# Optimization experiments

Measured on AMD Instinct MI355X. Metric: run time of the kernel, lower is better.

## Reference

```python
import jax, jax.numpy as jnp
import numpy as np

B, C, D, H, W = 2, 128, 16, 16, 16
NH = 4
HD = C // NH
GROUPS = 32
EPS = 1e-5


def group_norm(x, w, b):
    # x: [B, C, D, H, W]; normalize over (C/GROUPS, D, H, W) per group
    Bb, Cc = x.shape[0], x.shape[1]
    xr = x.reshape(Bb, GROUPS, -1)
    mu = xr.mean(axis=-1, keepdims=True)
    var = xr.var(axis=-1, keepdims=True)
    xn = ((xr - mu) * jax.lax.rsqrt(var + EPS)).reshape(x.shape)
    return xn * w.reshape(1, Cc, 1, 1, 1) + b.reshape(1, Cc, 1, 1, 1)


def setup_inputs() -> dict:
    key = jax.random.key(0)
    k0, k1, k2 = jax.random.split(key, 3)
    x = jax.random.normal(k0, (B, C, D, H, W), dtype=jnp.float32)
    gn_w = jnp.ones((C,), dtype=jnp.float32)
    gn_b = jnp.zeros((C,), dtype=jnp.float32)
    # 1x1x1 Conv3d weights as [out_ch, in_ch] matrices
    qkv_w = jax.random.normal(k1, (3 * C, C), dtype=jnp.float32) / np.sqrt(C).astype(np.float32)
    qkv_b = jnp.zeros((3 * C,), dtype=jnp.float32)
    out_w = jax.random.normal(k2, (C, C), dtype=jnp.float32) / np.sqrt(C).astype(np.float32)
    out_b = jnp.zeros((C,), dtype=jnp.float32)
    return {"x": x, "gn_w": gn_w, "gn_b": gn_b, "qkv_w": qkv_w, "qkv_b": qkv_b,
            "out_w": out_w, "out_b": out_b}


def reference(x, gn_w, gn_b, qkv_w, qkv_b, out_w, out_b):
    Bb, Cc, Dd, Hh, Ww = x.shape
    N = Dd * Hh * Ww
    scale = HD ** (-0.5)

    xn = group_norm(x, gn_w, gn_b)
    xf = xn.reshape(Bb, Cc, N)                              # [B, C, N]
    qkv = jnp.einsum('oc,bcn->bon', qkv_w, xf) + qkv_b[None, :, None]
    qkv = qkv.reshape(Bb, 3, NH, HD, N)
    q, k, v = qkv[:, 0], qkv[:, 1], qkv[:, 2]               # each [B, h, hd, N]

    attn = jnp.einsum('bhdn,bhdm->bhnm', q, k) * scale      # [B, h, N, N]
    attn = jax.nn.softmax(attn, axis=-1)
    o = jnp.einsum('bhnm,bhdm->bhdn', attn, v)              # [B, h, hd, N]
    o = o.reshape(Bb, Cc, N)

    y = jnp.einsum('oc,bcn->bon', out_w, o) + out_b[None, :, None]
    return y.reshape(Bb, Cc, Dd, Hh, Ww) + x
```

## Files before the change

### kernel.cpp

```cpp
#include <hip/hip_runtime.h>
#include <hip/hip_bf16.h>

#define B_ 2
#define C_ 128
#define N_ 4096
#define NH_ 4
#define HD_ 32
#define GROUPS_ 32
#define EPS_ 1e-5f
#define SCALE2_ 0.25503486f
#define NCH_ 4
#define CHKV_ 1024
#define NT_ (CHKV_ / 64)

typedef __attribute__((ext_vector_type(4))) float f32x4;
typedef __attribute__((ext_vector_type(8))) short s16x8;
typedef __attribute__((ext_vector_type(2))) unsigned int u32x2;
typedef __attribute__((ext_vector_type(4))) unsigned int u32x4;
typedef unsigned short u16;
typedef unsigned int u32;

static __device__ __forceinline__ u32 cvtpk_bf16(float lo, float hi) {
  u32 r;
  asm("v_cvt_pk_bf16_f32 %0, %1, %2" : "=v"(r) : "v"(lo), "v"(hi));
  return r;
}
static __device__ __forceinline__ float fexp2(float x) {
  float r;
  asm("v_exp_f32 %0, %1" : "=v"(r) : "v"(x));
  return r;
}
static __device__ __forceinline__ float bflo(u32 w) { return __uint_as_float(w << 16); }
static __device__ __forceinline__ float bfhi(u32 w) { return __uint_as_float(w & 0xffff0000u); }

__global__ __launch_bounds__(256) void k_groupnorm(
    const float* __restrict__ x, const float* __restrict__ gw,
    const float* __restrict__ gb, u16* __restrict__ xn) {
  const int blk = blockIdx.x;
  const int tid = threadIdx.x;
  const size_t base = (size_t)blk * (4 * N_);
  const f32x4* x4 = (const f32x4*)(x + base);
  float s = 0.f, ss = 0.f;
  for (int i = tid; i < 4096; i += 256) {
    f32x4 v = x4[i];
    s  += v.x + v.y + v.z + v.w;
    ss += v.x*v.x + v.y*v.y + v.z*v.z + v.w*v.w;
  }
  for (int off = 32; off; off >>= 1) {
    s  += __shfl_down(s, off);
    ss += __shfl_down(ss, off);
  }
  __shared__ float red[2][4];
  __shared__ float mv[2];
  const int wid = tid >> 6;
  if ((tid & 63) == 0) { red[0][wid] = s; red[1][wid] = ss; }
  __syncthreads();
  if (tid == 0) {
    float S = red[0][0]+red[0][1]+red[0][2]+red[0][3];
    float Q = red[1][0]+red[1][1]+red[1][2]+red[1][3];
    float mu  = S * (1.f/16384.f);
    float var = Q * (1.f/16384.f) - mu*mu;
    mv[0] = mu; mv[1] = rsqrtf(var + EPS_);
  }
  __syncthreads();
  const float mu = mv[0], rs = mv[1];
  const int gi = blk & (GROUPS_ - 1);
  u32x2* xn2 = (u32x2*)(xn + base);
  for (int i = tid; i < 4096; i += 256) {
    const int c = gi*4 + (i >> 10);
    const float a  = gw[c] * rs;
    const float b2 = gb[c] - mu * a;
    f32x4 v = x4[i];
    f32x4 r = v * a + b2;
    u32x2 p = { cvtpk_bf16(r.x, r.y), cvtpk_bf16(r.z, r.w) };
    xn2[i] = p;
  }
}

__global__ __launch_bounds__(256) void k_gemm_qkv(
    const u16* __restrict__ xn, const float* __restrict__ w,
    const float* __restrict__ bias, u16* __restrict__ out) {
  const int tid = threadIdx.x;
  const int n0 = blockIdx.x * 1024 + tid * 4;
  const int o0 = blockIdx.y * 8;
  const int b  = blockIdx.z;
  const u16* xb = xn + (size_t)b * C_ * N_;
  const float* wp = w + (size_t)o0 * C_;
  f32x4 a0 = {0.f,0.f,0.f,0.f}, a1 = a0, a2 = a0, a3 = a0;
  f32x4 a4 = a0, a5 = a0, a6 = a0, a7 = a0;
  #pragma unroll 4
  for (int c = 0; c < C_; ++c) {
    const u32* xr = (const u32*)(xb + (size_t)c * N_ + n0);
    const u32 lo = xr[0], hi = xr[1];
    const f32x4 xv = { bflo(lo), bfhi(lo), bflo(hi), bfhi(hi) };
    a0 += xv * wp[c];
    a1 += xv * wp[C_ + c];
    a2 += xv * wp[2*C_ + c];
    a3 += xv * wp[3*C_ + c];
    a4 += xv * wp[4*C_ + c];
    a5 += xv * wp[5*C_ + c];
    a6 += xv * wp[6*C_ + c];
    a7 += xv * wp[7*C_ + c];
  }
  const float sc = (o0 < 128) ? SCALE2_ : 1.0f;
  u16* op = out + ((size_t)b * 384 + o0) * N_ + n0;
  f32x4 acc[8] = {a0,a1,a2,a3,a4,a5,a6,a7};
  #pragma unroll
  for (int i = 0; i < 8; ++i) {
    f32x4 r = (acc[i] + bias[o0 + i]) * sc;
    u32x2 p = { cvtpk_bf16(r.x, r.y), cvtpk_bf16(r.z, r.w) };
    *(u32x2*)(op + (size_t)i * N_) = p;
  }
}

__global__ __launch_bounds__(256) void k_conv_k(
    const u16* __restrict__ qkvb, u16* __restrict__ Kt) {
  __shared__ u16 T[32][136];
  const int m0 = blockIdx.x * 128;
  const int h = blockIdx.y, b = blockIdx.z;
  const int tid = threadIdx.x;
  const u16* kb = qkvb + ((size_t)b * 384 + 128 + h * HD_) * N_;
  #pragma unroll
  for (int rep = 0; rep < 2; ++rep) {
    const int idx = rep * 256 + tid;
    const int dd = idx >> 4, mm = (idx & 15) * 8;
    *(s16x8*)&T[dd][mm] = *(const s16x8*)(kb + (size_t)dd * N_ + m0 + mm);
  }
  __syncthreads();
  u16* kout = Kt + ((size_t)(b * NH_ + h) * N_ + m0) * HD_;
  #pragma unroll
  for (int rep = 0; rep < 2; ++rep) {
    const int idx = rep * 256 + tid;
    const int mm = idx >> 2, d8 = (idx & 3) * 8;
    u32x4 pk;
    pk.x = (u32)T[d8][mm]   | ((u32)T[d8+1][mm] << 16);
    pk.y = (u32)T[d8+2][mm] | ((u32)T[d8+3][mm] << 16);
    pk.z = (u32)T[d8+4][mm] | ((u32)T[d8+5][mm] << 16);
    pk.w = (u32)T[d8+6][mm] | ((u32)T[d8+7][mm] << 16);
    *(u32x4*)(kout + (size_t)mm * HD_ + d8) = pk;
  }
}

__global__ __launch_bounds__(256) void k_attn(
    const u16* __restrict__ qkvb, const u16* __restrict__ Kt,
    float* __restrict__ Opart, float* __restrict__ Lpart) {
  __shared__ u16 Kl[64 * 32];
  __shared__ u16 Vl[32 * 72];
  const int b = blockIdx.z, h = blockIdx.y;
  const int qt = blockIdx.x & 31, ch = blockIdx.x >> 5;
  const int tid = threadIdx.x;
  const int wid = tid >> 6, lane = tid & 63;
  const int g = lane >> 4, lq = lane & 15;
  const int q0 = qt * 128 + wid * 16;
  const int kv0 = ch * CHKV_;

  const u16* qb = qkvb + ((size_t)b * 384 + h * HD_) * N_;
  s16x8 qfA, qfB;
  #pragma unroll
  for (int j = 0; j < 8; ++j) {
    qfA[j] = (short)qb[(size_t)(8*g + j) * N_ + q0 + lq];
    qfB[j] = (short)qb[(size_t)(8*g + j) * N_ + q0 + 64 + lq];
  }

  const u16* ktb = Kt + (size_t)(b * NH_ + h) * N_ * HD_;
  const u16* vbb = qkvb + ((size_t)b * 384 + 256 + h * HD_) * N_;
  const int pi = ((lq >> 2) << 3) + (lq & 3);

  const u16* kst = ktb + (size_t)kv0 * HD_ + tid * 8;
  const int vrow = tid >> 3;
  const int vcol = (tid & 7) * 8;
  const u16* vst = vbb + (size_t)vrow * N_ + kv0 + vcol;
  u16* kdst = Kl + ((tid * 8) ^ (((tid >> 5) & 3) * 8));
  u16* vdst = Vl + vrow * 72 + vcol;

  const int xsw  = (pi >> 3) & 3;
  const int slot = 8 * (g ^ xsw);
  const int ka0 = (pi)      * 32 + slot;
  const int ka1 = (pi + 4)  * 32 + slot;
  const int ka2 = (pi + 32) * 32 + slot;
  const int ka3 = (pi + 36) * 32 + slot;
  const int va0 = lq * 72 + 8*g;
  const int va1 = (lq + 16) * 72 + 8*g;

  const short one_bf = (short)0x3F80;
  const s16x8 onesB = {one_bf, one_bf, one_bf, one_bf,
                       one_bf, one_bf, one_bf, one_bf};

  f32x4 oa0A = {0.f,0.f,0.f,0.f}, oa1A = oa0A, oLA = oa0A;
  f32x4 oa0B = oa0A, oa1B = oa0A, oLB = oa0A;

  {
    s16x8 kr = *(const s16x8*)(kst);
    s16x8 vr = *(const s16x8*)(vst);
    *(s16x8*)(kdst) = kr;
    *(s16x8*)(vdst) = vr;
  }
  __syncthreads();

  for (int tt = 0; tt < NT_; ++tt) {
    const int tn = (tt + 1 < NT_) ? (tt + 1) : (NT_ - 1);
    s16x8 kr = *(const s16x8*)(kst + (size_t)tn * 64 * HD_);
    s16x8 vr = *(const s16x8*)(vst + (size_t)tn * 64);

    const s16x8 ck0 = *(const s16x8*)(Kl + ka0);
    const s16x8 ck1 = *(const s16x8*)(Kl + ka1);
    const s16x8 ck2 = *(const s16x8*)(Kl + ka2);
    const s16x8 ck3 = *(const s16x8*)(Kl + ka3);
    const s16x8 cv0 = *(const s16x8*)(Vl + va0);
    const s16x8 cv1 = *(const s16x8*)(Vl + va1);
    const s16x8 cv2 = *(const s16x8*)(Vl + va0 + 32);
    const s16x8 cv3 = *(const s16x8*)(Vl + va1 + 32);

    const f32x4 z = {0.f,0.f,0.f,0.f};
    {
      f32x4 s0 = __builtin_amdgcn_mfma_f32_16x16x32_bf16(ck0, qfA, z, 0, 0, 0);
      f32x4 s1 = __builtin_amdgcn_mfma_f32_16x16x32_bf16(ck1, qfA, z, 0, 0, 0);
      f32x4 s2 = __builtin_amdgcn_mfma_f32_16x16x32_bf16(ck2, qfA, z, 0, 0, 0);
      f32x4 s3 = __builtin_amdgcn_mfma_f32_16x16x32_bf16(ck3, qfA, z, 0, 0, 0);
      float p0 = fexp2(s0.x), p1 = fexp2(s0.y), p2 = fexp2(s0.z), p3 = fexp2(s0.w);
      float p4 = fexp2(s1.x), p5 = fexp2(s1.y), p6 = fexp2(s1.z), p7 = fexp2(s1.w);
      float p8 = fexp2(s2.x), p9 = fexp2(s2.y), pa_ = fexp2(s2.z), pb_ = fexp2(s2.w);
      float pc_ = fexp2(s3.x), pd_ = fexp2(s3.y), pe_ = fexp2(s3.z), pf_ = fexp2(s3.w);
      union { u32x4 u; s16x8 s; } pkA, pkB;
      pkA.u.x = cvtpk_bf16(p0, p1);   pkA.u.y = cvtpk_bf16(p2, p3);
      pkA.u.z = cvtpk_bf16(p4, p5);   pkA.u.w = cvtpk_bf16(p6, p7);
      pkB.u.x = cvtpk_bf16(p8, p9);   pkB.u.y = cvtpk_bf16(pa_, pb_);
      pkB.u.z = cvtpk_bf16(pc_, pd_); pkB.u.w = cvtpk_bf16(pe_, pf_);
      oa0A = __builtin_amdgcn_mfma_f32_16x16x32_bf16(pkA.s, cv0, oa0A, 0, 0, 0);
      oa1A = __builtin_amdgcn_mfma_f32_16x16x32_bf16(pkA.s, cv1, oa1A, 0, 0, 0);
      oLA  = __builtin_amdgcn_mfma_f32_16x16x32_bf16(pkA.s, onesB, oLA, 0, 0, 0);
      oa0A = __builtin_amdgcn_mfma_f32_16x16x32_bf16(pkB.s, cv2, oa0A, 0, 0, 0);
      oa1A = __builtin_amdgcn_mfma_f32_16x16x32_bf16(pkB.s, cv3, oa1A, 0, 0, 0);
      oLA  = __builtin_amdgcn_mfma_f32_16x16x32_bf16(pkB.s, onesB, oLA, 0, 0, 0);
    }
    {
      f32x4 s0 = __builtin_amdgcn_mfma_f32_16x16x32_bf16(ck0, qfB, z, 0, 0, 0);
      f32x4 s1 = __builtin_amdgcn_mfma_f32_16x16x32_bf16(ck1, qfB, z, 0, 0, 0);
      f32x4 s2 = __builtin_amdgcn_mfma_f32_16x16x32_bf16(ck2, qfB, z, 0, 0, 0);
      f32x4 s3 = __builtin_amdgcn_mfma_f32_16x16x32_bf16(ck3, qfB, z, 0, 0, 0);
      float p0 = fexp2(s0.x), p1 = fexp2(s0.y), p2 = fexp2(s0.z), p3 = fexp2(s0.w);
      float p4 = fexp2(s1.x), p5 = fexp2(s1.y), p6 = fexp2(s1.z), p7 = fexp2(s1.w);
      float p8 = fexp2(s2.x), p9 = fexp2(s2.y), pa_ = fexp2(s2.z), pb_ = fexp2(s2.w);
      float pc_ = fexp2(s3.x), pd_ = fexp2(s3.y), pe_ = fexp2(s3.z), pf_ = fexp2(s3.w);
      union { u32x4 u; s16x8 s; } pkA, pkB;
      pkA.u.x = cvtpk_bf16(p0, p1);   pkA.u.y = cvtpk_bf16(p2, p3);
      pkA.u.z = cvtpk_bf16(p4, p5);   pkA.u.w = cvtpk_bf16(p6, p7);
      pkB.u.x = cvtpk_bf16(p8, p9);   pkB.u.y = cvtpk_bf16(pa_, pb_);
      pkB.u.z = cvtpk_bf16(pc_, pd_); pkB.u.w = cvtpk_bf16(pe_, pf_);
      oa0B = __builtin_amdgcn_mfma_f32_16x16x32_bf16(pkA.s, cv0, oa0B, 0, 0, 0);
      oa1B = __builtin_amdgcn_mfma_f32_16x16x32_bf16(pkA.s, cv1, oa1B, 0, 0, 0);
      oLB  = __builtin_amdgcn_mfma_f32_16x16x32_bf16(pkA.s, onesB, oLB, 0, 0, 0);
      oa0B = __builtin_amdgcn_mfma_f32_16x16x32_bf16(pkB.s, cv2, oa0B, 0, 0, 0);
      oa1B = __builtin_amdgcn_mfma_f32_16x16x32_bf16(pkB.s, cv3, oa1B, 0, 0, 0);
      oLB  = __builtin_amdgcn_mfma_f32_16x16x32_bf16(pkB.s, onesB, oLB, 0, 0, 0);
    }

    __syncthreads();
    *(s16x8*)(kdst) = kr;
    *(s16x8*)(vdst) = vr;
    __syncthreads();
  }

  const int bh = b * NH_ + h;
  float* opb = Opart + ((size_t)ch * (B_ * NH_) + bh) * ((size_t)N_ * HD_);
  #pragma unroll
  for (int r = 0; r < 4; ++r) {
    const int qrow = q0 + g*4 + r;
    opb[(size_t)qrow * HD_ + lq]             = oa0A[r];
    opb[(size_t)qrow * HD_ + lq + 16]        = oa1A[r];
    opb[(size_t)(qrow + 64) * HD_ + lq]      = oa0B[r];
    opb[(size_t)(qrow + 64) * HD_ + lq + 16] = oa1B[r];
  }
  if (lq == 0) {
    float* lp = Lpart + ((size_t)ch * (B_ * NH_) + bh) * N_ + q0 + g*4;
    lp[0] = oLA[0]; lp[1] = oLA[1]; lp[2] = oLA[2]; lp[3] = oLA[3];
    lp[64] = oLB[0]; lp[65] = oLB[1]; lp[66] = oLB[2]; lp[67] = oLB[3];
  }
}

__global__ __launch_bounds__(256) void k_comb(
    const float* __restrict__ Opart, const float* __restrict__ Lpart,
    u16* __restrict__ O) {
  __shared__ float T[32][65];
  __shared__ float linv[64];
  const int t = threadIdx.x;
  const int nt = blockIdx.x & 63, bh = blockIdx.x >> 6;
  const int n0 = nt * 64;
  const float* opb = Opart + (size_t)bh * ((size_t)N_ * HD_) + (size_t)n0 * HD_;

  f32x4 acc0 = {0.f,0.f,0.f,0.f}, acc1 = acc0;
  #pragma unroll
  for (int c = 0; c < NCH_; ++c) {
    const float* p = opb + (size_t)c * ((size_t)B_ * NH_ * N_ * HD_);
    acc0 += *(const f32x4*)(p + (size_t)t * 4);
    acc1 += *(const f32x4*)(p + (size_t)(t + 256) * 4);
  }
  if (t < 64) {
    float s = 0.f;
    #pragma unroll
    for (int c = 0; c < NCH_; ++c)
      s += Lpart[((size_t)c * (B_ * NH_) + bh) * N_ + n0 + t];
    linv[t] = 1.0f / s;
  }
  __syncthreads();
  {
    int nl = t >> 3, d0 = (t & 7) * 4;
    float iv = linv[nl];
    T[d0][nl] = acc0.x*iv; T[d0+1][nl] = acc0.y*iv;
    T[d0+2][nl] = acc0.z*iv; T[d0+3][nl] = acc0.w*iv;
    nl = (t + 256) >> 3; d0 = (t & 7) * 4;
    iv = linv[nl];
    T[d0][nl] = acc1.x*iv; T[d0+1][nl] = acc1.y*iv;
    T[d0+2][nl] = acc1.z*iv; T[d0+3][nl] = acc1.w*iv;
  }
  __syncthreads();
  u16* ob = O + (size_t)bh * (HD_ * N_) + n0;
  const int row = t >> 3, col = (t & 7) * 8;
  u32x4 pk = { cvtpk_bf16(T[row][col],   T[row][col+1]),
               cvtpk_bf16(T[row][col+2], T[row][col+3]),
               cvtpk_bf16(T[row][col+4], T[row][col+5]),
               cvtpk_bf16(T[row][col+6], T[row][col+7]) };
  *(u32x4*)(ob + (size_t)row * N_ + col) = pk;
}

__global__ __launch_bounds__(256) void k_gemm_out(
    const u16* __restrict__ O, const float* __restrict__ w,
    const float* __restrict__ bias, const float* __restrict__ x,
    float* __restrict__ y) {
  const int tid = threadIdx.x;
  const int n0 = blockIdx.x * 1024 + tid * 4;
  const int o0 = blockIdx.y * 4;
  const int b  = blockIdx.z;
  const u16* ob = O + (size_t)b * C_ * N_;
  const float* wp = w + (size_t)o0 * C_;
  f32x4 a0 = {0.f,0.f,0.f,0.f}, a1 = a0, a2 = a0, a3 = a0;
  #pragma unroll 4
  for (int c = 0; c < C_; ++c) {
    const u32* xr = (const u32*)(ob + (size_t)c * N_ + n0);
    const u32 lo = xr[0], hi = xr[1];
    const f32x4 xv = { bflo(lo), bfhi(lo), bflo(hi), bfhi(hi) };
    a0 += xv * wp[c];
    a1 += xv * wp[C_ + c];
    a2 += xv * wp[2*C_ + c];
    a3 += xv * wp[3*C_ + c];
  }
  const size_t yo = ((size_t)b * C_ + o0) * N_ + n0;
  *(f32x4*)(y + yo)        = a0 + bias[o0]   + *(const f32x4*)(x + yo);
  *(f32x4*)(y + yo + N_)   = a1 + bias[o0+1] + *(const f32x4*)(x + yo + N_);
  *(f32x4*)(y + yo + 2*N_) = a2 + bias[o0+2] + *(const f32x4*)(x + yo + 2*N_);
  *(f32x4*)(y + yo + 3*N_) = a3 + bias[o0+3] + *(const f32x4*)(x + yo + 3*N_);
}

extern "C" void kernel_launch(void* const* d_in, const int* in_sizes, int n_in,
                              void* d_out, int out_size, void* d_ws, size_t ws_size,
                              hipStream_t stream) {
  const float* x     = (const float*)d_in[0];
  const float* gn_w  = (const float*)d_in[1];
  const float* gn_b  = (const float*)d_in[2];
  const float* qkv_w = (const float*)d_in[3];
  const float* qkv_b = (const float*)d_in[4];
  const float* out_w = (const float*)d_in[5];
  const float* out_b = (const float*)d_in[6];
  float* y = (float*)d_out;

  float* ws  = (float*)d_ws;
  u16*   xn   = (u16*)ws;
  u16*   qkvb = (u16*)(ws + 524288);
  u16*   Kt   = (u16*)(ws + 2097152);
  float* Opart = ws + 2621440;
  float* Lpart = ws + 6815744;
  u16*   O    = qkvb;

  k_groupnorm<<<dim3(B_ * GROUPS_), 256, 0, stream>>>(x, gn_w, gn_b, xn);
  k_gemm_qkv <<<dim3(4, 48, B_),    256, 0, stream>>>(xn, qkv_w, qkv_b, qkvb);
  k_conv_k   <<<dim3(32, NH_, B_),  256, 0, stream>>>(qkvb, Kt);
  k_attn     <<<dim3(32 * NCH_, NH_, B_), 256, 0, stream>>>(qkvb, Kt, Opart, Lpart);
  k_comb     <<<dim3(512),          256, 0, stream>>>(Opart, Lpart, O);
  k_gemm_out <<<dim3(4, 32, B_),    256, 0, stream>>>(O, out_w, out_b, x, y);
}
```

Baseline: 85.43 us.

## Fuse K transpose into QKV GEMM epilogue and halve per-thread column work

The QKV projection now writes K directly in the transposed [bh, N, HD] layout from its epilogue, removing the separate k_conv_k launch and its round trip through global memory. Both the QKV and output GEMMs process 2 columns per thread instead of 4, doubling grid size to improve occupancy and latency hiding on the many-CU device. In exchange, each weight scalar load is amortised over fewer outputs and global loads and stores become narrower, and the K stores are strided 16-byte writes.

New measurement: 79.80 us. -6.6%, faster.

```diff
diff --git a/kernel.cpp b/kernel.cpp
--- a/kernel.cpp
+++ b/kernel.cpp
@@ -13,6 +13,7 @@
 #define CHKV_ 1024
 #define NT_ (CHKV_ / 64)
 
+typedef __attribute__((ext_vector_type(2))) float f32x2;
 typedef __attribute__((ext_vector_type(4))) float f32x4;
 typedef __attribute__((ext_vector_type(8))) short s16x8;
 typedef __attribute__((ext_vector_type(2))) unsigned int u32x2;
@@ -79,65 +80,52 @@
 
 __global__ __launch_bounds__(256) void k_gemm_qkv(
     const u16* __restrict__ xn, const float* __restrict__ w,
-    const float* __restrict__ bias, u16* __restrict__ out) {
+    const float* __restrict__ bias, u16* __restrict__ qkvb,
+    u16* __restrict__ Kt) {
   const int tid = threadIdx.x;
-  const int n0 = blockIdx.x * 1024 + tid * 4;
+  const int n0 = blockIdx.x * 512 + tid * 2;
   const int o0 = blockIdx.y * 8;
   const int b  = blockIdx.z;
   const u16* xb = xn + (size_t)b * C_ * N_;
   const float* wp = w + (size_t)o0 * C_;
-  f32x4 a0 = {0.f,0.f,0.f,0.f}, a1 = a0, a2 = a0, a3 = a0;
-  f32x4 a4 = a0, a5 = a0, a6 = a0, a7 = a0;
+  float ax[8] = {0,0,0,0,0,0,0,0};
+  float ay[8] = {0,0,0,0,0,0,0,0};
   #pragma unroll 4
   for (int c = 0; c < C_; ++c) {
-    const u32* xr = (const u32*)(xb + (size_t)c * N_ + n0);
-    const u32 lo = xr[0], hi = xr[1];
-    const f32x4 xv = { bflo(lo), bfhi(lo), bflo(hi), bfhi(hi) };
-    a0 += xv * wp[c];
-    a1 += xv * wp[C_ + c];
-    a2 += xv * wp[2*C_ + c];
-    a3 += xv * wp[3*C_ + c];
-    a4 += xv * wp[4*C_ + c];
-    a5 += xv * wp[5*C_ + c];
-    a6 += xv * wp[6*C_ + c];
-    a7 += xv * wp[7*C_ + c];
-  }
-  const float sc = (o0 < 128) ? SCALE2_ : 1.0f;
-  u16* op = out + ((size_t)b * 384 + o0) * N_ + n0;
-  f32x4 acc[8] = {a0,a1,a2,a3,a4,a5,a6,a7};
+    const u32 wv = *(const u32*)(xb + (size_t)c * N_ + n0);
+    const float x0 = bflo(wv), x1 = bfhi(wv);
+    #pragma unroll
+    for (int i = 0; i < 8; ++i) {
+      const float wi = wp[(size_t)i * C_ + c];
+      ax[i] += x0 * wi;
+      ay[i] += x1 * wi;
+    }
+  }
   #pragma unroll
   for (int i = 0; i < 8; ++i) {
-    f32x4 r = (acc[i] + bias[o0 + i]) * sc;
-    u32x2 p = { cvtpk_bf16(r.x, r.y), cvtpk_bf16(r.z, r.w) };
-    *(u32x2*)(op + (size_t)i * N_) = p;
-  }
-}
-
-__global__ __launch_bounds__(256) void k_conv_k(
-    const u16* __restrict__ qkvb, u16* __restrict__ Kt) {
-  __shared__ u16 T[32][136];
-  const int m0 = blockIdx.x * 128;
-  const int h = blockIdx.y, b = blockIdx.z;
-  const int tid = threadIdx.x;
-  const u16* kb = qkvb + ((size_t)b * 384 + 128 + h * HD_) * N_;
-  #pragma unroll
-  for (int rep = 0; rep < 2; ++rep) {
-    const int idx = rep * 256 + tid;
-    const int dd = idx >> 4, mm = (idx & 15) * 8;
-    *(s16x8*)&T[dd][mm] = *(const s16x8*)(kb + (size_t)dd * N_ + m0 + mm);
-  }
-  __syncthreads();
-  u16* kout = Kt + ((size_t)(b * NH_ + h) * N_ + m0) * HD_;
-  #pragma unroll
-  for (int rep = 0; rep < 2; ++rep) {
-    const int idx = rep * 256 + tid;
-    const int mm = idx >> 2, d8 = (idx & 3) * 8;
-    u32x4 pk;
-    pk.x = (u32)T[d8][mm]   | ((u32)T[d8+1][mm] << 16);
-    pk.y = (u32)T[d8+2][mm] | ((u32)T[d8+3][mm] << 16);
-    pk.z = (u32)T[d8+4][mm] | ((u32)T[d8+5][mm] << 16);
-    pk.w = (u32)T[d8+6][mm] | ((u32)T[d8+7][mm] << 16);
-    *(u32x4*)(kout + (size_t)mm * HD_ + d8) = pk;
+    const float bi = bias[o0 + i];
+    ax[i] += bi; ay[i] += bi;
+  }
+  if (o0 < 128) {
+    u16* op = qkvb + ((size_t)b * 384 + o0) * N_ + n0;
+    #pragma unroll
+    for (int i = 0; i < 8; ++i)
+      *(u32*)(op + (size_t)i * N_) = cvtpk_bf16(ax[i] * SCALE2_, ay[i] * SCALE2_);
+  } else if (o0 < 256) {
+    const int h  = (o0 - 128) >> 5;
+    const int d8 = (o0 - 128) & 31;
+    u16* kb = Kt + (size_t)(b * NH_ + h) * N_ * HD_ + d8;
+    u32x4 pk0 = { cvtpk_bf16(ax[0], ax[1]), cvtpk_bf16(ax[2], ax[3]),
+                  cvtpk_bf16(ax[4], ax[5]), cvtpk_bf16(ax[6], ax[7]) };
+    u32x4 pk1 = { cvtpk_bf16(ay[0], ay[1]), cvtpk_bf16(ay[2], ay[3]),
+                  cvtpk_bf16(ay[4], ay[5]), cvtpk_bf16(ay[6], ay[7]) };
+    *(u32x4*)(kb + (size_t)n0 * HD_)       = pk0;
+    *(u32x4*)(kb + (size_t)(n0 + 1) * HD_) = pk1;
+  } else {
+    u16* op = qkvb + ((size_t)b * 384 + o0) * N_ + n0;
+    #pragma unroll
+    for (int i = 0; i < 8; ++i)
+      *(u32*)(op + (size_t)i * N_) = cvtpk_bf16(ax[i], ay[i]);
   }
 }
 
@@ -328,27 +316,31 @@
     const float* __restrict__ bias, const float* __restrict__ x,
     float* __restrict__ y) {
   const int tid = threadIdx.x;
-  const int n0 = blockIdx.x * 1024 + tid * 4;
+  const int n0 = blockIdx.x * 512 + tid * 2;
   const int o0 = blockIdx.y * 4;
   const int b  = blockIdx.z;
   const u16* ob = O + (size_t)b * C_ * N_;
   const float* wp = w + (size_t)o0 * C_;
-  f32x4 a0 = {0.f,0.f,0.f,0.f}, a1 = a0, a2 = a0, a3 = a0;
+  float ax[4] = {0,0,0,0};
+  float ay[4] = {0,0,0,0};
   #pragma unroll 4
   for (int c = 0; c < C_; ++c) {
-    const u32* xr = (const u32*)(ob + (size_t)c * N_ + n0);
-    const u32 lo = xr[0], hi = xr[1];
-    const f32x4 xv = { bflo(lo), bfhi(lo), bflo(hi), bfhi(hi) };
-    a0 += xv * wp[c];
-    a1 += xv * wp[C_ + c];
-    a2 += xv * wp[2*C_ + c];
-    a3 += xv * wp[3*C_ + c];
+    const u32 wv = *(const u32*)(ob + (size_t)c * N_ + n0);
+    const float x0 = bflo(wv), x1 = bfhi(wv);
+    #pragma unroll
+    for (int i = 0; i < 4; ++i) {
+      const float wi = wp[(size_t)i * C_ + c];
+      ax[i] += x0 * wi;
+      ay[i] += x1 * wi;
+    }
   }
   const size_t yo = ((size_t)b * C_ + o0) * N_ + n0;
-  *(f32x4*)(y + yo)        = a0 + bias[o0]   + *(const f32x4*)(x + yo);
-  *(f32x4*)(y + yo + N_)   = a1 + bias[o0+1] + *(const f32x4*)(x + yo + N_);
-  *(f32x4*)(y + yo + 2*N_) = a2 + bias[o0+2] + *(const f32x4*)(x + yo + 2*N_);
-  *(f32x4*)(y + yo + 3*N_) = a3 + bias[o0+3] + *(const f32x4*)(x + yo + 3*N_);
+  #pragma unroll
+  for (int i = 0; i < 4; ++i) {
+    const f32x2 xr = *(const f32x2*)(x + yo + (size_t)i * N_);
+    f32x2 r = { ax[i] + bias[o0+i] + xr.x, ay[i] + bias[o0+i] + xr.y };
+    *(f32x2*)(y + yo + (size_t)i * N_) = r;
+  }
 }
 
 extern "C" void kernel_launch(void* const* d_in, const int* in_sizes, int n_in,
@@ -372,9 +364,8 @@
   u16*   O    = qkvb;
 
   k_groupnorm<<<dim3(B_ * GROUPS_), 256, 0, stream>>>(x, gn_w, gn_b, xn);
-  k_gemm_qkv <<<dim3(4, 48, B_),    256, 0, stream>>>(xn, qkv_w, qkv_b, qkvb);
-  k_conv_k   <<<dim3(32, NH_, B_),  256, 0, stream>>>(qkvb, Kt);
+  k_gemm_qkv <<<dim3(8, 48, B_),    256, 0, stream>>>(xn, qkv_w, qkv_b, qkvb, Kt);
   k_attn     <<<dim3(32 * NCH_, NH_, B_), 256, 0, stream>>>(qkvb, Kt, Opart, Lpart);
   k_comb     <<<dim3(512),          256, 0, stream>>>(Opart, Lpart, O);
-  k_gemm_out <<<dim3(4, 32, B_),    256, 0, stream>>>(O, out_w, out_b, x, y);
-}
+  k_gemm_out <<<dim3(8, 32, B_),    256, 0, stream>>>(O, out_w, out_b, x, y);
+}
```
